# Performance work log

Hardware: AMD Instinct MI355X
Metric: run time of the kernel (lower is better)

Reference implementation:

```python
import jax, jax.numpy as jnp
import numpy as np

FORWARD_STEPS = 300


def setup_inputs() -> dict:
    key = jax.random.key(0)
    k1, k2, k3, k4 = jax.random.split(key, 4)
    B, T, F = 1024, 2048, 16
    return {
        "vi": jax.random.uniform(k1, (B,), dtype=jnp.float32),
        "delta_y": jax.random.uniform(k2, (B,), dtype=jnp.float32),
        "v_previous": jax.random.uniform(k3, (B,), dtype=jnp.float32),
        "x_input": jax.random.uniform(k4, (B, T, F), dtype=jnp.float32),
        "w": jnp.asarray(4.1, dtype=jnp.float32),  # learned scalar, init Constant(4.1)
    }


def _newell_forward(x_input, w, forward_steps):
    B, T, F = x_input.shape
    x_last = x_input[:, -1, :]                     # [B, F]
    i_idx = jnp.arange(forward_steps, dtype=jnp.float32)  # [S]

    temps, valids = [], []
    for j in (1, 2, 3, 4):  # unrolled while_loop body, j=1..4
        d = jnp.sum(x_last[:, :j], axis=-1)        # [B]
        td = d * 150.0 / (w + x_last[:, 4 + j] * 25.0)  # [B]
        # referred_index = cast(i - td*10, int32) then clip to [0, T-1]
        ref = (i_idx[:, None] - (td * 10.0)[None, :]).astype(jnp.int32)  # [S, B]
        ref = jnp.clip(ref, 0, T - 1)
        feat = x_input[:, :, 9 + j]                # [B, T]
        temp = jnp.take_along_axis(feat, ref.T, axis=1).T  # [S, B]
        temps.append(temp)
        valids.append(jnp.any(temp != 0, axis=1))  # [S] — reduce_any over batch

    temps = jnp.stack(temps, axis=1)               # [S, 4, B]
    valid = jnp.stack(valids, axis=1)              # [S, 4]
    # early-exit semantics: ahat = temp of FIRST j with any nonzero, else zeros
    sel = jnp.argmax(valid, axis=1)                # [S]
    ahat = jnp.take_along_axis(temps, sel[:, None, None], axis=1)[:, 0, :]  # [S, B]
    ahat = jnp.where(jnp.any(valid, axis=1)[:, None], ahat, jnp.float32(0.0))
    return ahat.T                                  # [B, S] == stack(predictions, axis=1)


def reference(vi, delta_y, v_previous, x_input, w):
    return _newell_forward(x_input, w, FORWARD_STEPS)
```

## Files before the change

kernel.cpp:

```cpp
#include <hip/hip_runtime.h>

#define T_DIM 2048
#define F_DIM 16
#define B_DIM 1024
#define STEPS 300

__global__ void k1_prep(const float* __restrict__ x, const float* __restrict__ wptr,
                        float* __restrict__ cbuf, unsigned* __restrict__ valid) {
#pragma clang fp contract(off)
    int b = blockIdx.x * blockDim.x + threadIdx.x;
    if (b < STEPS) valid[b] = 0u;
    if (b >= B_DIM) return;
    const float* xl = x + ((size_t)b * T_DIM + (T_DIM - 1)) * F_DIM;
    float w = *wptr;
    float d = 0.0f;
#pragma unroll
    for (int j0 = 0; j0 < 4; ++j0) {
        d = d + xl[j0];
        float den = w + xl[5 + j0] * 25.0f;
        float td  = (d * 150.0f) / den;
        cbuf[j0 * B_DIM + b] = td * 10.0f;
    }
}

__global__ void k2_valid(const float* __restrict__ x, const float* __restrict__ cbuf,
                         unsigned* __restrict__ valid) {
#pragma clang fp contract(off)
    int i = blockIdx.x;
    int b = blockIdx.y * blockDim.x + threadIdx.x;
    unsigned m = 0;
#pragma unroll
    for (int j0 = 0; j0 < 4; ++j0) {
        float c = cbuf[j0 * B_DIM + b];
        int idx = (int)((float)i - c);
        idx = idx < 0 ? 0 : (idx > T_DIM - 1 ? T_DIM - 1 : idx);
        float v = x[((size_t)b * T_DIM + idx) * F_DIM + 10 + j0];
        if (v != 0.0f) m |= 1u << j0;
    }
    unsigned wm = 0;
#pragma unroll
    for (int j0 = 0; j0 < 4; ++j0) {
        if (__ballot((m >> j0) & 1u) != 0ull) wm |= 1u << j0;
    }
    if ((threadIdx.x & 63) == 0 && wm) atomicOr(&valid[i], wm);
}

__global__ void k3_out(const float* __restrict__ x, const float* __restrict__ cbuf,
                       const unsigned* __restrict__ valid, float* __restrict__ out) {
#pragma clang fp contract(off)
    int g = blockIdx.x * blockDim.x + threadIdx.x;
    if (g >= B_DIM * STEPS) return;
    int b = g / STEPS;
    int i = g - b * STEPS;
    unsigned m = valid[i];
    float r = 0.0f;
    if (m) {
        int j0 = __ffs(m) - 1;
        float c = cbuf[j0 * B_DIM + b];
        int idx = (int)((float)i - c);
        idx = idx < 0 ? 0 : (idx > T_DIM - 1 ? T_DIM - 1 : idx);
        r = x[((size_t)b * T_DIM + idx) * F_DIM + 10 + j0];
    }
    out[g] = r;
}

extern "C" void kernel_launch(void* const* d_in, const int* in_sizes, int n_in,
                              void* d_out, int out_size, void* d_ws, size_t ws_size,
                              hipStream_t stream) {
    const float* x    = (const float*)d_in[3];
    const float* wptr = (const float*)d_in[4];
    float* out = (float*)d_out;

    float*    cbuf  = (float*)d_ws;
    unsigned* valid = (unsigned*)((char*)d_ws + 4 * B_DIM * sizeof(float));

    hipLaunchKernelGGL(k1_prep, dim3(4), dim3(256), 0, stream, x, wptr, cbuf, valid);
    hipLaunchKernelGGL(k2_valid, dim3(STEPS, 4), dim3(256), 0, stream, x, cbuf, valid);
    hipLaunchKernelGGL(k3_out, dim3((B_DIM * STEPS + 255) / 256), dim3(256), 0, stream,
                       x, cbuf, valid, out);
}
```

Before: 184.8 us.

## Compact gathered features and nonzero bitmasks before validity and output passes

Adds a first pass that copies features 10-13 for the first 300 timesteps into a compact per-(j,b) buffer and builds per-wave nonzero bitmasks. The validity pass then tests bits in these masks instead of gathering from the strided input, and the output pass reads from the compact buffer. Indices are clamped to 299 rather than T-1, relying on the fact that i minus a nonnegative offset never exceeds 299. This removes scattered 64-byte-stride reads across the large input, at the cost of an extra write pass and more workspace.

```diff
diff --git a/kernel.cpp b/kernel.cpp
--- a/kernel.cpp
+++ b/kernel.cpp
@@ -4,62 +4,119 @@
 #define F_DIM 16
 #define B_DIM 1024
 #define STEPS 300
+#define TC 304
 
-__global__ void k1_prep(const float* __restrict__ x, const float* __restrict__ wptr,
-                        float* __restrict__ cbuf, unsigned* __restrict__ valid) {
+#define OFF_CBUF  (4u * B_DIM * TC * 4u)
+#define OFF_NZ    (OFF_CBUF + 4u * B_DIM * 4u)
+#define OFF_VALID (OFF_NZ + 4u * B_DIM * 5u * 8u)
+
+__global__ void __launch_bounds__(320) kA(const float* __restrict__ x,
+                                          const float* __restrict__ wptr,
+                                          float* __restrict__ F,
+                                          float* __restrict__ cbuf,
+                                          unsigned long long* __restrict__ NZ,
+                                          unsigned long long* __restrict__ validw) {
 #pragma clang fp contract(off)
-    int b = blockIdx.x * blockDim.x + threadIdx.x;
-    if (b < STEPS) valid[b] = 0u;
-    if (b >= B_DIM) return;
-    const float* xl = x + ((size_t)b * T_DIM + (T_DIM - 1)) * F_DIM;
-    float w = *wptr;
-    float d = 0.0f;
+    int b = blockIdx.x;
+    int t = threadIdx.x;
+    if (b == 0 && t < 20) validw[t] = 0ull;
+
+    if (t == 0) {
+        const float* xl = x + ((size_t)b * T_DIM + (T_DIM - 1)) * F_DIM;
+        float w = *wptr;
+        float d = 0.0f;
 #pragma unroll
-    for (int j0 = 0; j0 < 4; ++j0) {
-        d = d + xl[j0];
-        float den = w + xl[5 + j0] * 25.0f;
-        float td  = (d * 150.0f) / den;
-        cbuf[j0 * B_DIM + b] = td * 10.0f;
+        for (int j0 = 0; j0 < 4; ++j0) {
+            d = d + xl[j0];
+            float den = w + xl[5 + j0] * 25.0f;
+            float td  = (d * 150.0f) / den;
+            cbuf[j0 * B_DIM + b] = td * 10.0f;
+        }
+    }
+
+    float v0 = 0.f, v1 = 0.f, v2 = 0.f, v3 = 0.f;
+    bool act = t < STEPS;
+    if (act) {
+        const float* row = x + ((size_t)b * T_DIM + t) * F_DIM;
+        float2 p0 = *(const float2*)(row + 10);
+        float2 p1 = *(const float2*)(row + 12);
+        v0 = p0.x; v1 = p0.y; v2 = p1.x; v3 = p1.y;
+        F[((size_t)(0 * B_DIM + b)) * TC + t] = v0;
+        F[((size_t)(1 * B_DIM + b)) * TC + t] = v1;
+        F[((size_t)(2 * B_DIM + b)) * TC + t] = v2;
+        F[((size_t)(3 * B_DIM + b)) * TC + t] = v3;
+    }
+    unsigned long long m0 = __ballot(act && v0 != 0.f);
+    unsigned long long m1 = __ballot(act && v1 != 0.f);
+    unsigned long long m2 = __ballot(act && v2 != 0.f);
+    unsigned long long m3 = __ballot(act && v3 != 0.f);
+    int w = t >> 6;
+    if ((t & 63) == 0) {
+        NZ[((size_t)(0 * B_DIM + b)) * 5 + w] = m0;
+        NZ[((size_t)(1 * B_DIM + b)) * 5 + w] = m1;
+        NZ[((size_t)(2 * B_DIM + b)) * 5 + w] = m2;
+        NZ[((size_t)(3 * B_DIM + b)) * 5 + w] = m3;
     }
 }
 
-__global__ void k2_valid(const float* __restrict__ x, const float* __restrict__ cbuf,
-                         unsigned* __restrict__ valid) {
+__global__ void __launch_bounds__(256) kB(const float* __restrict__ cbuf,
+                                          const unsigned long long* __restrict__ NZ,
+                                          unsigned long long* __restrict__ validw) {
 #pragma clang fp contract(off)
-    int i = blockIdx.x;
-    int b = blockIdx.y * blockDim.x + threadIdx.x;
-    unsigned m = 0;
+    int tid = blockIdx.x * 256 + threadIdx.x;
+    int b  = tid & 1023;
+    int wj = tid >> 10;
+    int j  = wj & 3;
+    int w  = wj >> 2;
+    float c = cbuf[j * B_DIM + b];
+    const unsigned long long* nzp = NZ + (size_t)(j * B_DIM + b) * 5;
+    unsigned long long nz0 = nzp[0], nz1 = nzp[1], nz2 = nzp[2], nz3 = nzp[3], nz4 = nzp[4];
+
+    unsigned long long a = 0;
+    int kmax = (w == 4) ? (STEPS - 256) : 64;
+    for (int k = 0; k < kmax; ++k) {
+        int i = w * 64 + k;
+        float r = (float)i - c;
+        int idx = (int)r;
+        idx = idx < 0 ? 0 : (idx > STEPS - 1 ? STEPS - 1 : idx);
+        unsigned long long word = idx < 64 ? nz0 : idx < 128 ? nz1 :
+                                  idx < 192 ? nz2 : idx < 256 ? nz3 : nz4;
+        a |= ((word >> (idx & 63)) & 1ull) << k;
+    }
+    unsigned lo = (unsigned)a, hi = (unsigned)(a >> 32);
 #pragma unroll
-    for (int j0 = 0; j0 < 4; ++j0) {
-        float c = cbuf[j0 * B_DIM + b];
-        int idx = (int)((float)i - c);
-        idx = idx < 0 ? 0 : (idx > T_DIM - 1 ? T_DIM - 1 : idx);
-        float v = x[((size_t)b * T_DIM + idx) * F_DIM + 10 + j0];
-        if (v != 0.0f) m |= 1u << j0;
+    for (int s = 32; s; s >>= 1) {
+        lo |= __shfl_xor(lo, s, 64);
+        hi |= __shfl_xor(hi, s, 64);
     }
-    unsigned wm = 0;
-#pragma unroll
-    for (int j0 = 0; j0 < 4; ++j0) {
-        if (__ballot((m >> j0) & 1u) != 0ull) wm |= 1u << j0;
+    if ((threadIdx.x & 63) == 0) {
+        unsigned long long red = ((unsigned long long)hi << 32) | lo;
+        if (red) atomicOr(&validw[j * 5 + w], red);
     }
-    if ((threadIdx.x & 63) == 0 && wm) atomicOr(&valid[i], wm);
 }
 
-__global__ void k3_out(const float* __restrict__ x, const float* __restrict__ cbuf,
-                       const unsigned* __restrict__ valid, float* __restrict__ out) {
+__global__ void __launch_bounds__(256) kC(const float* __restrict__ F,
+                                          const float* __restrict__ cbuf,
+                                          const unsigned long long* __restrict__ validw,
+                                          float* __restrict__ out) {
 #pragma clang fp contract(off)
-    int g = blockIdx.x * blockDim.x + threadIdx.x;
+    int g = blockIdx.x * 256 + threadIdx.x;
     if (g >= B_DIM * STEPS) return;
     int b = g / STEPS;
     int i = g - b * STEPS;
-    unsigned m = valid[i];
+    int wi = i >> 6, bi = i & 63;
+    unsigned m = 0;
+#pragma unroll
+    for (int j = 0; j < 4; ++j)
+        m |= (unsigned)((validw[j * 5 + wi] >> bi) & 1ull) << j;
     float r = 0.0f;
     if (m) {
-        int j0 = __ffs(m) - 1;
-        float c = cbuf[j0 * B_DIM + b];
-        int idx = (int)((float)i - c);
-        idx = idx < 0 ? 0 : (idx > T_DIM - 1 ? T_DIM - 1 : idx);
-        r = x[((size_t)b * T_DIM + idx) * F_DIM + 10 + j0];
+        int j = __ffs(m) - 1;
+        float c = cbuf[j * B_DIM + b];
+        float rr = (float)i - c;
+        int idx = (int)rr;
+        idx = idx < 0 ? 0 : (idx > STEPS - 1 ? STEPS - 1 : idx);
+        r = F[(size_t)(j * B_DIM + b) * TC + idx];
     }
     out[g] = r;
 }
@@ -71,11 +128,13 @@
     const float* wptr = (const float*)d_in[4];
     float* out = (float*)d_out;
 
-    float*    cbuf  = (float*)d_ws;
-    unsigned* valid = (unsigned*)((char*)d_ws + 4 * B_DIM * sizeof(float));
+    float*              Fbuf   = (float*)d_ws;
+    float*              cbuf   = (float*)((char*)d_ws + OFF_CBUF);
+    unsigned long long* NZ     = (unsigned long long*)((char*)d_ws + OFF_NZ);
+    unsigned long long* validw = (unsigned long long*)((char*)d_ws + OFF_VALID);
 
-    hipLaunchKernelGGL(k1_prep, dim3(4), dim3(256), 0, stream, x, wptr, cbuf, valid);
-    hipLaunchKernelGGL(k2_valid, dim3(STEPS, 4), dim3(256), 0, stream, x, cbuf, valid);
-    hipLaunchKernelGGL(k3_out, dim3((B_DIM * STEPS + 255) / 256), dim3(256), 0, stream,
-                       x, cbuf, valid, out);
+    hipLaunchKernelGGL(kA, dim3(B_DIM), dim3(320), 0, stream, x, wptr, Fbuf, cbuf, NZ, validw);
+    hipLaunchKernelGGL(kB, dim3(80), dim3(256), 0, stream, cbuf, NZ, validw);
+    hipLaunchKernelGGL(kC, dim3((B_DIM * STEPS + 255) / 256), dim3(256), 0, stream,
+                       Fbuf, cbuf, validw, out);
 }
```

After: 186.7 us. About the same (+1.0%).
